# Kernel tuning notes

Hardware: AMD Instinct MI355X
Metric: run time of the kernel (lower is better)

Reference implementation:

```python
import jax, jax.numpy as jnp
import numpy as np
import math

B, L, D_IN = 4, 8192, 64
H = 256          # d_model
N2 = 32          # d_state // 2 complex conjugate pairs (S4D)
NL = 4           # n_layers
D_OUT = 10


def setup_inputs() -> dict:
    key = jax.random.key(0)
    ks = jax.random.split(key, 16)
    x = jax.random.normal(ks[0], (B, L, D_IN), dtype=jnp.float32)
    # encoder Linear(d_input, d_model)
    enc_W = jax.random.normal(ks[1], (H, D_IN), dtype=jnp.float32) / np.sqrt(D_IN)
    enc_b = jnp.zeros((H,), dtype=jnp.float32)
    # per-layer S4D parameters (stacked over n_layers)
    log_dt = jax.random.uniform(ks[2], (NL, H), dtype=jnp.float32,
                                minval=math.log(1e-3), maxval=math.log(1e-1))
    log_A_re = jnp.full((NL, H, N2), math.log(0.5), dtype=jnp.float32)
    A_im = jnp.tile(math.pi * jnp.arange(N2, dtype=jnp.float32), (NL, H, 1))
    C_re = jax.random.normal(ks[3], (NL, H, N2), dtype=jnp.float32) * (0.5 ** 0.5)
    C_im = jax.random.normal(ks[4], (NL, H, N2), dtype=jnp.float32) * (0.5 ** 0.5)
    D = jax.random.normal(ks[5], (NL, H), dtype=jnp.float32)
    # S4 block output linear (H -> 2H) followed by GLU
    Wo = jax.random.normal(ks[6], (NL, 2 * H, H), dtype=jnp.float32) / np.sqrt(H)
    bo = jnp.zeros((NL, 2 * H), dtype=jnp.float32)
    # post-norm LayerNorm over d_model
    ln_w = jnp.ones((NL, H), dtype=jnp.float32)
    ln_b = jnp.zeros((NL, H), dtype=jnp.float32)
    # final decoder Linear(d_model, d_output)
    out_W = jax.random.normal(ks[7], (D_OUT, H), dtype=jnp.float32) / np.sqrt(H)
    out_b = jnp.zeros((D_OUT,), dtype=jnp.float32)
    return dict(x=x, enc_W=enc_W, enc_b=enc_b, log_dt=log_dt, log_A_re=log_A_re,
                A_im=A_im, C_re=C_re, C_im=C_im, D=D, Wo=Wo, bo=bo,
                ln_w=ln_w, ln_b=ln_b, out_W=out_W, out_b=out_b)


def _s4d_kernel(log_dt, log_A_re, A_im, C_re, C_im, L):
    # S4D-ZOH-ish (S4D-Lin) kernel: K[h,l] = 2 Re sum_n C~[h,n] exp(l*dt*A[h,n])
    dt = jnp.exp(log_dt)[:, None]                      # (H,1)
    A = -jnp.exp(log_A_re) + 1j * A_im                 # (H,N2)
    dtA = dt * A                                       # (H,N2)
    Ct = (C_re + 1j * C_im) * (jnp.exp(dtA) - 1.0) / A # (H,N2)
    t = jnp.arange(L, dtype=jnp.float32)
    V = jnp.exp(dtA[:, :, None] * t)                   # (H,N2,L) Vandermonde
    return 2.0 * jnp.einsum('hn,hnl->hl', Ct, V).real  # (H,L)


def reference(x, enc_W, enc_b, log_dt, log_A_re, A_im, C_re, C_im, D, Wo, bo,
              ln_w, ln_b, out_W, out_b):
    Bc, Lc, _ = x.shape
    h = x @ enc_W.T + enc_b          # (B,L,H)
    h = h.transpose(0, 2, 1)         # (B,H,L) (transposed layout)
    n_layers = log_dt.shape[0]
    for i in range(n_layers):
        K = _s4d_kernel(log_dt[i], log_A_re[i], A_im[i], C_re[i], C_im[i], Lc)
        # FFT convolution (causal, non-circular via 2L padding)
        Kf = jnp.fft.rfft(K, n=2 * Lc)                       # (H, L+1)
        hf = jnp.fft.rfft(h, n=2 * Lc)                       # (B,H,L+1)
        y = jnp.fft.irfft(hf * Kf, n=2 * Lc)[..., :Lc]
        y = y + D[i][:, None] * h                            # skip D*u
        y = jax.nn.gelu(y)
        # output linear (H -> 2H) + GLU, pointwise over length
        u = jnp.einsum('oh,bhl->bol', Wo[i], y) + bo[i][:, None]
        Hd = h.shape[1]
        z = u[:, :Hd] * jax.nn.sigmoid(u[:, Hd:])
        h = z + h                                            # residual
        # post-norm LayerNorm over channel (d_model) dim
        mu = h.mean(axis=1, keepdims=True)
        var = h.var(axis=1, keepdims=True)
        h = (h - mu) / jnp.sqrt(var + 1e-5) * ln_w[i][:, None] + ln_b[i][:, None]
    h = h.transpose(0, 2, 1)          # (B,L,H)
    return h @ out_W.T + out_b        # (B,L,d_output)
```

## Files before the change

### kernel.cpp

```cpp
#include <hip/hip_runtime.h>
#include <hip/hip_bf16.h>


constexpr int B_ = 4, L_ = 8192, DIN = 64, H_ = 256, N2_ = 32, NL_ = 4, DOUT = 10;
constexpr int LC = 64, CHK = L_ / LC;
constexpr int GCH = B_ * CHK;
constexpr int M_ = B_ * L_;

constexpr size_t OFF_WOB  = 8388608;
constexpr size_t OFF_PW   = 8650752;
constexpr size_t OFF_PCT  = 8716288;
constexpr size_t OFF_PWLC = 8781824;
constexpr size_t OFF_PZ   = 8847360;
constexpr size_t OFF_EWT  = 8912896;
constexpr size_t OFF_UCM  = 8929280;
constexpr size_t OFF_YCM  = 13123584;
constexpr size_t OFF_MT   = 21512192;
constexpr size_t OFF_MW   = 22036480;
constexpr size_t OFF_MV   = 22560768;

typedef short bf16x8 __attribute__((ext_vector_type(8)));
typedef short short8 __attribute__((ext_vector_type(8)));
typedef float f32x4  __attribute__((ext_vector_type(4)));
typedef int   int2v  __attribute__((ext_vector_type(2)));

__device__ __forceinline__ float b2f(short s) {
    union { float f; unsigned u; } c;
    c.u = ((unsigned)(unsigned short)s) << 16;
    return c.f;
}

__global__ __launch_bounds__(256) void k_params(
    const float* __restrict__ log_dt, const float* __restrict__ log_A_re,
    const float* __restrict__ A_im, const float* __restrict__ C_re,
    const float* __restrict__ C_im, float* __restrict__ ws)
{
    int idx = blockIdx.x * 256 + threadIdx.x;
    if (idx >= NL_ * H_ * N2_) return;
    int i  = idx / (H_ * N2_);
    int hh = (idx / N2_) % H_;
    float dt  = expf(log_dt[i * H_ + hh]);
    float Are = -expf(log_A_re[idx]);
    float Aim = A_im[idx];
    float zre = dt * Are, zim = dt * Aim;
    float er  = expf(zre);
    float wre = er * cosf(zim), wim = er * sinf(zim);
    float d   = Are * Are + Aim * Aim;
    float nre = wre - 1.f, nim = wim;
    float qre = (nre * Are + nim * Aim) / d;
    float qim = (nim * Are - nre * Aim) / d;
    float cr = C_re[idx], ci = C_im[idx];
    float ctre = cr * qre - ci * qim;
    float ctim = cr * qim + ci * qre;
    float er2 = expf(zre * (float)LC);
    float wlre = er2 * cosf(zim * (float)LC);
    float wlim = er2 * sinf(zim * (float)LC);
    ((float2*)(ws + OFF_PW))[idx]   = make_float2(wre, wim);
    ((float2*)(ws + OFF_PCT))[idx]  = make_float2(2.f * ctre, 2.f * ctim);
    ((float2*)(ws + OFF_PWLC))[idx] = make_float2(wlre, wlim);
    ((float2*)(ws + OFF_PZ))[idx]   = make_float2(zre, zim);
}

__global__ __launch_bounds__(256) void k_mats(const float* __restrict__ ws,
    int layer, __hip_bfloat16* __restrict__ mt, __hip_bfloat16* __restrict__ mw,
    __hip_bfloat16* __restrict__ mv)
{
    int h = blockIdx.x, tid = threadIdx.x;
    __shared__ float zre[32], zim[32], ctr[32], cti[32], kv[64];
    if (tid < 32) {
        float2 z = ((const float2*)(ws + OFF_PZ))[(size_t)layer*H_*N2_ + h*N2_ + tid];
        float2 c = ((const float2*)(ws + OFF_PCT))[(size_t)layer*H_*N2_ + h*N2_ + tid];
        zre[tid] = z.x; zim[tid] = z.y; ctr[tid] = c.x; cti[tid] = c.y;
    }
    __syncthreads();
    if (tid < 64) {
        float d = (float)tid, acc = 0.f;
        for (int n = 0; n < 32; n++) {
            float er = expf(zre[n] * d);
            float co = cosf(zim[n] * d), si = sinf(zim[n] * d);
            acc += er * (ctr[n] * co - cti[n] * si);
        }
        kv[tid] = acc;
    }
    __syncthreads();
    {
        int t = tid >> 2, j0 = (tid & 3) * 16;
        alignas(16) __hip_bfloat16 row[16];
        #pragma unroll
        for (int jj = 0; jj < 16; jj++) {
            int j = j0 + jj;
            row[jj] = __float2bfloat16(j <= t ? kv[t - j] : 0.f);
        }
        *(short8*)(mt + (size_t)h*4096 + t*64 + j0)     = *(short8*)&row[0];
        *(short8*)(mt + (size_t)h*4096 + t*64 + j0 + 8) = *(short8*)&row[8];
    }
    {
        int n = tid >> 3, j0 = (tid & 7) * 8;
        alignas(16) __hip_bfloat16 rre[8], rim[8];
        #pragma unroll
        for (int jj = 0; jj < 8; jj++) {
            float e = (float)(63 - (j0 + jj));
            float er = expf(zre[n] * e);
            rre[jj] = __float2bfloat16(er * cosf(zim[n] * e));
            rim[jj] = __float2bfloat16(er * sinf(zim[n] * e));
        }
        *(short8*)(mw + (size_t)h*4096 + (2*n)*64 + j0)   = *(short8*)&rre[0];
        *(short8*)(mw + (size_t)h*4096 + (2*n+1)*64 + j0) = *(short8*)&rim[0];
    }
    {
        int t = tid >> 2, n0 = (tid & 3) * 8;
        float e = (float)(t + 1);
        alignas(16) __hip_bfloat16 row[16];
        #pragma unroll
        for (int k = 0; k < 8; k++) {
            int n = n0 + k;
            float er = expf(zre[n] * e);
            float wr = er * cosf(zim[n] * e), wi = er * sinf(zim[n] * e);
            row[2*k]   = __float2bfloat16(ctr[n]*wr - cti[n]*wi);
            row[2*k+1] = __float2bfloat16(-(ctr[n]*wi + cti[n]*wr));
        }
        *(short8*)(mv + (size_t)h*4096 + t*64 + 2*n0)     = *(short8*)&row[0];
        *(short8*)(mv + (size_t)h*4096 + t*64 + 2*n0 + 8) = *(short8*)&row[8];
    }
}

__global__ __launch_bounds__(256) void k_transpose(const float* __restrict__ src,
    float* __restrict__ dst, int R, int Cc)
{
    __shared__ float t[32][33];
    int x = blockIdx.x * 32 + threadIdx.x;
    #pragma unroll
    for (int i = 0; i < 4; i++) {
        int yy = blockIdx.y * 32 + threadIdx.y + i * 8;
        if (x < Cc && yy < R) t[threadIdx.y + i * 8][threadIdx.x] = src[(size_t)yy * Cc + x];
    }
    __syncthreads();
    int xo = blockIdx.y * 32 + threadIdx.x;
    #pragma unroll
    for (int i = 0; i < 4; i++) {
        int yo = blockIdx.x * 32 + threadIdx.y + i * 8;
        if (xo < R && yo < Cc) dst[(size_t)yo * R + xo] = t[threadIdx.x][threadIdx.y + i * 8];
    }
}

__global__ __launch_bounds__(256) void k_wcvt(const float* __restrict__ src,
    __hip_bfloat16* __restrict__ dst, int n4)
{
    int i = blockIdx.x * 256 + threadIdx.x;
    if (i >= n4) return;
    float4 v = ((const float4*)src)[i];
    union { __hip_bfloat16 b[4]; uint2 u; } o;
    o.b[0] = __float2bfloat16(v.x); o.b[1] = __float2bfloat16(v.y);
    o.b[2] = __float2bfloat16(v.z); o.b[3] = __float2bfloat16(v.w);
    ((uint2*)dst)[i] = o.u;
}

__global__ __launch_bounds__(256) void k_encoder(const float* __restrict__ x,
    const float* __restrict__ encWT, const float* __restrict__ enc_b,
    __hip_bfloat16* __restrict__ u)
{
    __shared__ float As[DIN][36];
    __shared__ float Bs[32][268];
    int m0e = blockIdx.x * 32;
    int tid = threadIdx.x;
    const float4* x4 = (const float4*)x;
    #pragma unroll
    for (int q = 0; q < 2; q++) {
        int f = tid * 2 + q;
        int row = f >> 4, kq = f & 15;
        float4 v = x4[(size_t)(m0e + row) * 16 + kq];
        As[kq * 4 + 0][row] = v.x; As[kq * 4 + 1][row] = v.y;
        As[kq * 4 + 2][row] = v.z; As[kq * 4 + 3][row] = v.w;
    }
    int tx = tid & 31, ty = tid >> 5;
    float acc[4][8];
    #pragma unroll
    for (int p = 0; p < 4; p++)
        #pragma unroll
        for (int j = 0; j < 8; j++) acc[p][j] = 0.f;
    const float4* w4 = (const float4*)encWT;
    for (int ks = 0; ks < 2; ks++) {
        __syncthreads();
        #pragma unroll
        for (int it = 0; it < 8; it++) {
            int q = it * 256 + tid;
            int row = q >> 6, c4 = q & 63;
            *(float4*)&Bs[row][c4 * 4] = w4[ks * 2048 + q];
        }
        __syncthreads();
        #pragma unroll 8
        for (int kk = 0; kk < 32; kk++) {
            int k = ks * 32 + kk;
            float4 a  = *(const float4*)&As[k][ty * 4];
            float4 b0 = *(const float4*)&Bs[kk][tx * 4];
            float4 b1 = *(const float4*)&Bs[kk][128 + tx * 4];
            float av[4] = {a.x, a.y, a.z, a.w};
            float bv[8] = {b0.x, b0.y, b0.z, b0.w, b1.x, b1.y, b1.z, b1.w};
            #pragma unroll
            for (int p = 0; p < 4; p++)
                #pragma unroll
                for (int j = 0; j < 8; j++)
                    acc[p][j] = fmaf(av[p], bv[j], acc[p][j]);
        }
    }
    float4 eb0 = *(const float4*)&enc_b[tx * 4];
    float4 eb1 = *(const float4*)&enc_b[128 + tx * 4];
    float ebv[8] = {eb0.x, eb0.y, eb0.z, eb0.w, eb1.x, eb1.y, eb1.z, eb1.w};
    __syncthreads();
    #pragma unroll
    for (int p = 0; p < 4; p++) {
        int pl = ty * 4 + p;
        #pragma unroll
        for (int j = 0; j < 4; j++) Bs[pl][tx * 4 + j]       = acc[p][j] + ebv[j];
        #pragma unroll
        for (int j = 0; j < 4; j++) Bs[pl][128 + tx * 4 + j] = acc[p][j + 4] + ebv[j + 4];
    }
    __syncthreads();
    {
        alignas(16) __hip_bfloat16 row[32];
        #pragma unroll
        for (int pl = 0; pl < 32; pl++) row[pl] = __float2bfloat16(Bs[pl][tid]);
        #pragma unroll
        for (int q = 0; q < 4; q++)
            *(short8*)(u + (size_t)tid * M_ + m0e + q * 8) = *(short8*)&row[q * 8];
    }
}

__global__ __launch_bounds__(256) void k_ssm(const __hip_bfloat16* __restrict__ ucm,
    const __hip_bfloat16* __restrict__ mt, const __hip_bfloat16* __restrict__ mw,
    const __hip_bfloat16* __restrict__ mv, const float* __restrict__ ws, int layer,
    const float* __restrict__ Dp, __hip_bfloat16* __restrict__ ycm)
{
    __shared__ __hip_bfloat16 ulds[L_];
    __shared__ __hip_bfloat16 st[CHK * 64];
    __shared__ float segT[8][32][2];
    int h = blockIdx.x >> 2, b = blockIdx.x & 3;
    int tid = threadIdx.x, w = tid >> 6, l = tid & 63, l15 = l & 15, l4 = l >> 4;
    const __hip_bfloat16* ub = ucm + (size_t)h * M_ + (size_t)b * L_;
    #pragma unroll
    for (int it = 0; it < 4; it++) {
        int e0 = it * 2048 + tid * 8;
        short8 v = *(const short8*)(ub + e0);
        int c = e0 >> 6, e = e0 & 63;
        *(short8*)&ulds[c * 64 + (e ^ ((c & 7) << 3))] = v;
    }
    __syncthreads();
    {
        const __hip_bfloat16* bbase = mw + (size_t)h * 4096 + l15 * 64 + l4 * 8;
        #pragma unroll
        for (int half = 0; half < 2; half++) {
            int g0 = (w + half * 4) * 16;
            int ca = g0 + l15;
            f32x4 acc[4];
            #pragma unroll
            for (int nj = 0; nj < 4; nj++) acc[nj] = (f32x4)0.f;
            #pragma unroll
            for (int ks = 0; ks < 2; ks++) {
                int e = l4 * 8 + ks * 32;
                bf16x8 a = *(const bf16x8*)&ulds[ca * 64 + (e ^ ((ca & 7) << 3))];
                #pragma unroll
                for (int nj = 0; nj < 4; nj++) {
                    bf16x8 bb = *(const bf16x8*)(bbase + nj * 16 * 64 + ks * 32);
                    acc[nj] = __builtin_amdgcn_mfma_f32_16x16x32_bf16(a, bb, acc[nj], 0, 0, 0);
                }
            }
            #pragma unroll
            for (int nj = 0; nj < 4; nj++)
                #pragma unroll
                for (int r = 0; r < 4; r++) {
                    int c = g0 + l4 * 4 + r, e = nj * 16 + l15;
                    st[c * 64 + (e ^ ((c & 7) << 3))] = __float2bfloat16(acc[nj][r]);
                }
        }
    }
    __syncthreads();
    {
        int s = tid >> 5, n = tid & 31;
        float2 wl = ((const float2*)(ws + OFF_PWLC))[(size_t)layer * H_ * N2_ + h * 32 + n];
        float tr = 0.f, ti = 0.f;
        for (int j = 0; j < 16; j++) {
            int c = s * 16 + j;
            __hip_bfloat162* p = (__hip_bfloat162*)&st[c * 64 + ((2 * n) ^ ((c & 7) << 3))];
            float2 v = __bfloat1622float2(*p);
            float nr = fmaf(wl.x, tr, v.x); nr = fmaf(-wl.y, ti, nr);
            float ni = fmaf(wl.x, ti, v.y); ni = fmaf(wl.y, tr, ni);
            tr = nr; ti = ni;
        }
        segT[s][n][0] = tr; segT[s][n][1] = ti;
        __syncthreads();
        float wr = wl.x, wi = wl.y;
        #pragma unroll
        for (int q = 0; q < 4; q++) {
            float nr = wr * wr - wi * wi, ni = 2.f * wr * wi;
            wr = nr; wi = ni;
        }
        float ar = 0.f, ai = 0.f;
        for (int t = 0; t < s; t++) {
            float Tx = segT[t][n][0], Ty = segT[t][n][1];
            float nr = fmaf(wr, ar, Tx); nr = fmaf(-wi, ai, nr);
            float ni = fmaf(wr, ai, Ty); ni = fmaf(wi, ar, ni);
            ar = nr; ai = ni;
        }
        for (int j = 0; j < 16; j++) {
            int c = s * 16 + j;
            __hip_bfloat162* p = (__hip_bfloat162*)&st[c * 64 + ((2 * n) ^ ((c & 7) << 3))];
            float2 v = __bfloat1622float2(*p);
            *p = __float22bfloat162_rn(make_float2(ar, ai));
            float nr = fmaf(wl.x, ar, v.x); nr = fmaf(-wl.y, ai, nr);
            float ni = fmaf(wl.x, ai, v.y); ni = fmaf(wl.y, ar, ni);
            ar = nr; ai = ni;
        }
    }
    __syncthreads();
    {
        const __hip_bfloat16* bt = mt + (size_t)h * 4096 + l15 * 64 + l4 * 8;
        const __hip_bfloat16* bv = mv + (size_t)h * 4096 + l15 * 64 + l4 * 8;
        float Dh = Dp[layer * H_ + h];
        __hip_bfloat16* yb = ycm + (size_t)h * M_ + (size_t)b * L_;
        #pragma unroll
        for (int half = 0; half < 2; half++) {
            int g0 = (w + half * 4) * 16;
            int ca = g0 + l15;
            f32x4 acc[4];
            #pragma unroll
            for (int nj = 0; nj < 4; nj++) acc[nj] = (f32x4)0.f;
            #pragma unroll
            for (int ks = 0; ks < 2; ks++) {
                int e = l4 * 8 + ks * 32;
                bf16x8 a = *(const bf16x8*)&ulds[ca * 64 + (e ^ ((ca & 7) << 3))];
                #pragma unroll
                for (int nj = 0; nj < 4; nj++) {
                    bf16x8 bb = *(const bf16x8*)(bt + nj * 16 * 64 + ks * 32);
                    acc[nj] = __builtin_amdgcn_mfma_f32_16x16x32_bf16(a, bb, acc[nj], 0, 0, 0);
                }
            }
            #pragma unroll
            for (int ks = 0; ks < 2; ks++) {
                int e = l4 * 8 + ks * 32;
                bf16x8 a = *(const bf16x8*)&st[ca * 64 + (e ^ ((ca & 7) << 3))];
                #pragma unroll
                for (int nj = 0; nj < 4; nj++) {
                    bf16x8 bb = *(const bf16x8*)(bv + nj * 16 * 64 + ks * 32);
                    acc[nj] = __builtin_amdgcn_mfma_f32_16x16x32_bf16(a, bb, acc[nj], 0, 0, 0);
                }
            }
            #pragma unroll
            for (int nj = 0; nj < 4; nj++)
                #pragma unroll
                for (int r = 0; r < 4; r++) {
                    int g = g0 + l4 * 4 + r;
                    int e = nj * 16 + l15;
                    float uv = __bfloat162float(ulds[g * 64 + (e ^ ((g & 7) << 3))]);
                    float v = fmaf(Dh, uv, acc[nj][r]);
                    float gg = 0.7978845608028654f * fmaf(0.044715f * v, v * v, v);
                    float yv = v / (1.f + __expf(-2.f * gg));
                    yb[(size_t)g * 64 + nj * 16 + l15] = __float2bfloat16(yv);
                }
        }
    }
}

__global__ __launch_bounds__(256) void k_glu_mfma(
    const __hip_bfloat16* __restrict__ ycm,
    const __hip_bfloat16* __restrict__ wob,
    const float* __restrict__ bo, const float* __restrict__ lnw,
    const float* __restrict__ lnb,
    __hip_bfloat16* __restrict__ u)
{
    __shared__ int buf[8320];
    __shared__ float red[4][32][2];
    int* bufA = buf;
    int* bufR = buf + 4160;
    int tid = threadIdx.x;
    int w = tid >> 6, l = tid & 63, l15 = l & 15, l4 = l >> 4;
    int mb = blockIdx.x * 64;
    int nv = w * 64;
    int p = tid & 127, ph = tid >> 7;
    const __hip_bfloat16* aB = ycm + (size_t)(2 * p) * M_ + mb + ph * 16;
    const __hip_bfloat16* rB = u + (size_t)(2 * p) * M_ + mb + ph * 16;

    short8 A0[4], R0[4], A1[4], R1[4];
    A0[0] = *(const short8*)(aB);          A0[1] = *(const short8*)(aB + 8);
    A0[2] = *(const short8*)(aB + M_);     A0[3] = *(const short8*)(aB + M_ + 8);
    R0[0] = *(const short8*)(rB);          R0[1] = *(const short8*)(rB + 8);
    R0[2] = *(const short8*)(rB + M_);     R0[3] = *(const short8*)(rB + M_ + 8);
    A1[0] = *(const short8*)(aB + 32);     A1[1] = *(const short8*)(aB + 40);
    A1[2] = *(const short8*)(aB + M_ + 32);A1[3] = *(const short8*)(aB + M_ + 40);

    float bov[4], bog[4], lw[4], lb[4];
    #pragma unroll
    for (int nj = 0; nj < 4; nj++) {
        int cn = nv + nj * 16 + l15;
        bov[nj] = bo[cn]; bog[nj] = bo[256 + cn];
        lw[nj] = lnw[cn]; lb[nj] = lnb[cn];
    }

    {
        int* da = bufA + ph * 16 * 130 + p;
        int* dr = bufR + ph * 16 * 130 + p;
        #pragma unroll
        for (int j = 0; j < 8; j++) {
            da[j * 130]       = ((int)(unsigned short)A0[0][j]) | (((int)(unsigned short)A0[2][j]) << 16);
            da[(8 + j) * 130] = ((int)(unsigned short)A0[1][j]) | (((int)(unsigned short)A0[3][j]) << 16);
            dr[j * 130]       = ((int)(unsigned short)R0[0][j]) | (((int)(unsigned short)R0[2][j]) << 16);
            dr[(8 + j) * 130] = ((int)(unsigned short)R0[1][j]) | (((int)(unsigned short)R0[3][j]) << 16);
        }
    }
    __syncthreads();

    int abase0 = l15 * 130 + l4 * 4;
    #pragma unroll
    for (int tile = 0; tile < 2; tile++) {
        int m0 = mb + tile * 32;
        f32x4 accv[2][4], accg[2][4];
        #pragma unroll
        for (int sub = 0; sub < 2; sub++)
            #pragma unroll
            for (int nj = 0; nj < 4; nj++) { accv[sub][nj] = (f32x4)0.f; accg[sub][nj] = (f32x4)0.f; }

        #pragma unroll 2
        for (int ks = 0; ks < 8; ks++) {
            int k0 = ks * 32 + l4 * 8;
            union { int2v d[2]; bf16x8 v; } a0u, a1u;
            a0u.d[0] = *(const int2v*)&bufA[abase0 + ks * 16];
            a0u.d[1] = *(const int2v*)&bufA[abase0 + ks * 16 + 2];
            a1u.d[0] = *(const int2v*)&bufA[abase0 + 16 * 130 + ks * 16];
            a1u.d[1] = *(const int2v*)&bufA[abase0 + 16 * 130 + ks * 16 + 2];
            bf16x8 a0 = a0u.v;
            bf16x8 a1 = a1u.v;
            #pragma unroll
            for (int nj = 0; nj < 4; nj++) {
                bf16x8 bv = *(const bf16x8*)(wob + (size_t)(nv + nj * 16 + l15) * H_ + k0);
                bf16x8 bg = *(const bf16x8*)(wob + (size_t)(256 + nv + nj * 16 + l15) * H_ + k0);
                accv[0][nj] = __builtin_amdgcn_mfma_f32_16x16x32_bf16(a0, bv, accv[0][nj], 0, 0, 0);
                accg[0][nj] = __builtin_amdgcn_mfma_f32_16x16x32_bf16(a0, bg, accg[0][nj], 0, 0, 0);
                accv[1][nj] = __builtin_amdgcn_mfma_f32_16x16x32_bf16(a1, bv, accv[1][nj], 0, 0, 0);
                accg[1][nj] = __builtin_amdgcn_mfma_f32_16x16x32_bf16(a1, bg, accg[1][nj], 0, 0, 0);
            }
        }

        const short* bufRs = (const short*)bufR;
        #pragma unroll
        for (int sub = 0; sub < 2; sub++) {
            #pragma unroll
            for (int r = 0; r < 4; r++) {
                int lr = sub * 16 + l4 * 4 + r;
                float s = 0.f, ss = 0.f;
                #pragma unroll
                for (int nj = 0; nj < 4; nj++) {
                    int cn = nv + nj * 16 + l15;
                    float uv = accv[sub][nj][r] + bov[nj];
                    float ug = accg[sub][nj][r] + bog[nj];
                    float z = uv / (1.f + __expf(-ug));
                    float v = z + b2f(bufRs[lr * 260 + cn]);
                    accv[sub][nj][r] = v;
                    s += v; ss += v * v;
                }
                #pragma unroll
                for (int off = 1; off < 16; off <<= 1) {
                    s  += __shfl_xor(s, off);
                    ss += __shfl_xor(ss, off);
                }
                if (l15 == 0) { red[w][lr][0] = s; red[w][lr][1] = ss; }
            }
        }
        if (tile == 0) {
            R1[0] = *(const short8*)(rB + 32);      R1[1] = *(const short8*)(rB + 40);
            R1[2] = *(const short8*)(rB + M_ + 32); R1[3] = *(const short8*)(rB + M_ + 40);
        }
        __syncthreads();
        short* lt = (short*)buf;
        #pragma unroll
        for (int sub = 0; sub < 2; sub++) {
            #pragma unroll
            for (int r = 0; r < 4; r++) {
                int lr = sub * 16 + l4 * 4 + r;
                float s  = red[0][lr][0] + red[1][lr][0] + red[2][lr][0] + red[3][lr][0];
                float ss = red[0][lr][1] + red[1][lr][1] + red[2][lr][1] + red[3][lr][1];
                float mu = s * (1.f / 256.f);
                float var = ss * (1.f / 256.f) - mu * mu;
                float rstd = rsqrtf(var + 1e-5f);
                #pragma unroll
                for (int nj = 0; nj < 4; nj++) {
                    int cn = nv + nj * 16 + l15;
                    float val = (accv[sub][nj][r] - mu) * rstd * lw[nj] + lb[nj];
                    __hip_bfloat16 bval = __float2bfloat16(val);
                    lt[cn * 34 + lr] = *(short*)&bval;
                }
            }
        }
        __syncthreads();
        #pragma unroll
        for (int q = 0; q < 4; q++)
            *(short8*)(u + (size_t)tid * M_ + m0 + q * 8)
                = *(short8*)&lt[tid * 34 + q * 8];
        if (tile == 0) {
            __syncthreads();
            int* da = bufA + ph * 16 * 130 + p;
            int* dr = bufR + ph * 16 * 130 + p;
            #pragma unroll
            for (int j = 0; j < 8; j++) {
                da[j * 130]       = ((int)(unsigned short)A1[0][j]) | (((int)(unsigned short)A1[2][j]) << 16);
                da[(8 + j) * 130] = ((int)(unsigned short)A1[1][j]) | (((int)(unsigned short)A1[3][j]) << 16);
                dr[j * 130]       = ((int)(unsigned short)R1[0][j]) | (((int)(unsigned short)R1[2][j]) << 16);
                dr[(8 + j) * 130] = ((int)(unsigned short)R1[1][j]) | (((int)(unsigned short)R1[3][j]) << 16);
            }
            __syncthreads();
        }
    }
}

__global__ __launch_bounds__(256) void k_decoder(const __hip_bfloat16* __restrict__ u,
    const float* __restrict__ out_W, const float* __restrict__ out_b,
    float* __restrict__ out)
{
    __shared__ int ds[64 * 130];
    __shared__ float wl[10][260];
    int m0 = blockIdx.x * 64;
    int tid = threadIdx.x;
    {
        int p = tid & 127, ph = tid >> 7;
        const __hip_bfloat16* s0 = u + (size_t)(2 * p) * M_ + m0 + ph * 32;
        const __hip_bfloat16* s1 = s0 + M_;
        short8 y0[4], y1[4];
        #pragma unroll
        for (int q = 0; q < 4; q++) {
            y0[q] = *(const short8*)(s0 + q * 8);
            y1[q] = *(const short8*)(s1 + q * 8);
        }
        int* dst = ds + (ph * 32) * 130 + p;
        #pragma unroll
        for (int q = 0; q < 4; q++)
            #pragma unroll
            for (int j = 0; j < 8; j++)
                dst[(q * 8 + j) * 130] =
                    ((int)(unsigned short)y0[q][j]) | (((int)(unsigned short)y1[q][j]) << 16);
    }
    for (int q = tid; q < 640; q += 256) {
        int r = q / 64, k4 = q % 64;
        *(float4*)&wl[r][k4 * 4] = ((const float4*)out_W)[q];
    }
    __syncthreads();
    int slot = tid & 15;
    if (slot < DOUT) {
        #pragma unroll
        for (int pass = 0; pass < 4; pass++) {
            int pl = pass * 16 + (tid >> 4);
            const int* row = ds + pl * 130;
            float a0 = 0.f, a1 = 0.f;
            #pragma unroll 8
            for (int d = 0; d < 128; d++) {
                int v = row[d];
                a0 = fmaf(b2f((short)(v & 0xffff)),  wl[slot][2 * d],     a0);
                a1 = fmaf(b2f((short)(v >> 16)),     wl[slot][2 * d + 1], a1);
            }
            out[(size_t)(m0 + pl) * DOUT + slot] = a0 + a1 + out_b[slot];
        }
    }
}

extern "C" void kernel_launch(void* const* d_in, const int* in_sizes, int n_in,
                              void* d_out, int out_size, void* d_ws, size_t ws_size,
                              hipStream_t stream)
{
    (void)in_sizes; (void)n_in; (void)out_size; (void)ws_size;
    const float* x        = (const float*)d_in[0];
    const float* enc_W    = (const float*)d_in[1];
    const float* enc_b    = (const float*)d_in[2];
    const float* log_dt   = (const float*)d_in[3];
    const float* log_A_re = (const float*)d_in[4];
    const float* A_im     = (const float*)d_in[5];
    const float* C_re     = (const float*)d_in[6];
    const float* C_im     = (const float*)d_in[7];
    const float* Dp       = (const float*)d_in[8];
    const float* Wo       = (const float*)d_in[9];
    const float* bo       = (const float*)d_in[10];
    const float* lnw      = (const float*)d_in[11];
    const float* lnb      = (const float*)d_in[12];
    const float* out_W    = (const float*)d_in[13];
    const float* out_b    = (const float*)d_in[14];
    float* ws = (float*)d_ws;
    __hip_bfloat16* u   = (__hip_bfloat16*)(ws + OFF_UCM);
    __hip_bfloat16* ycm = (__hip_bfloat16*)(ws + OFF_YCM);
    __hip_bfloat16* mt = (__hip_bfloat16*)(ws + OFF_MT);
    __hip_bfloat16* mw = (__hip_bfloat16*)(ws + OFF_MW);
    __hip_bfloat16* mv = (__hip_bfloat16*)(ws + OFF_MV);
    __hip_bfloat16* wob = (__hip_bfloat16*)(ws + OFF_WOB);

    k_params<<<NL_ * H_ * N2_ / 256, 256, 0, stream>>>(log_dt, log_A_re, A_im, C_re, C_im, ws);
    dim3 tb(32, 8);
    k_transpose<<<dim3(DIN / 32, H_ / 32), tb, 0, stream>>>(enc_W, ws + OFF_EWT, H_, DIN);
    k_wcvt<<<(NL_ * 2 * H_ * H_ / 4 + 255) / 256, 256, 0, stream>>>(Wo, wob, NL_ * 2 * H_ * H_ / 4);
    k_encoder<<<M_ / 32, 256, 0, stream>>>(x, ws + OFF_EWT, enc_b, u);
    for (int i = 0; i < NL_; i++) {
        k_mats<<<H_, 256, 0, stream>>>(ws, i, mt, mw, mv);
        k_ssm<<<H_ * B_, 256, 0, stream>>>(u, mt, mw, mv, ws, i, Dp, ycm);
        k_glu_mfma<<<M_ / 64, 256, 0, stream>>>(ycm,
            wob + (size_t)i * 2 * H_ * H_, bo + (size_t)i * 2 * H_,
            lnw + (size_t)i * H_, lnb + (size_t)i * H_, u);
    }
    k_decoder<<<M_ / 64, 256, 0, stream>>>(u, out_W, out_b, (float*)d_out);
}
```

Before: 418.8 us.

## Use bf16 MFMA for encoder and batch SSM matrix generation across layers

```diff
diff --git a/kernel.cpp b/kernel.cpp
--- a/kernel.cpp
+++ b/kernel.cpp
@@ -7,17 +7,18 @@
 constexpr int GCH = B_ * CHK;
 constexpr int M_ = B_ * L_;
 
+constexpr size_t OFF_XB   = 0;
+constexpr size_t OFF_EWB  = 1048576;
 constexpr size_t OFF_WOB  = 8388608;
 constexpr size_t OFF_PW   = 8650752;
 constexpr size_t OFF_PCT  = 8716288;
 constexpr size_t OFF_PWLC = 8781824;
 constexpr size_t OFF_PZ   = 8847360;
-constexpr size_t OFF_EWT  = 8912896;
 constexpr size_t OFF_UCM  = 8929280;
 constexpr size_t OFF_YCM  = 13123584;
-constexpr size_t OFF_MT   = 21512192;
-constexpr size_t OFF_MW   = 22036480;
-constexpr size_t OFF_MV   = 22560768;
+constexpr size_t OFF_MTA  = 17317888;
+constexpr size_t OFF_MWA  = 19415040;
+constexpr size_t OFF_MVA  = 21512192;
 
 typedef short bf16x8 __attribute__((ext_vector_type(8)));
 typedef short short8 __attribute__((ext_vector_type(8)));
@@ -61,15 +62,18 @@
     ((float2*)(ws + OFF_PZ))[idx]   = make_float2(zre, zim);
 }
 
-__global__ __launch_bounds__(256) void k_mats(const float* __restrict__ ws,
-    int layer, __hip_bfloat16* __restrict__ mt, __hip_bfloat16* __restrict__ mw,
+__global__ __launch_bounds__(256) void k_mats_all(const float* __restrict__ ws,
+    __hip_bfloat16* __restrict__ mt, __hip_bfloat16* __restrict__ mw,
     __hip_bfloat16* __restrict__ mv)
 {
-    int h = blockIdx.x, tid = threadIdx.x;
+    int bid = blockIdx.x;
+    int layer = bid >> 8, h = bid & 255;
+    int lh = layer * H_ + h;
+    int tid = threadIdx.x;
     __shared__ float zre[32], zim[32], ctr[32], cti[32], kv[64];
     if (tid < 32) {
-        float2 z = ((const float2*)(ws + OFF_PZ))[(size_t)layer*H_*N2_ + h*N2_ + tid];
-        float2 c = ((const float2*)(ws + OFF_PCT))[(size_t)layer*H_*N2_ + h*N2_ + tid];
+        float2 z = ((const float2*)(ws + OFF_PZ))[(size_t)lh * N2_ + tid];
+        float2 c = ((const float2*)(ws + OFF_PCT))[(size_t)lh * N2_ + tid];
         zre[tid] = z.x; zim[tid] = z.y; ctr[tid] = c.x; cti[tid] = c.y;
     }
     __syncthreads();
@@ -91,8 +95,8 @@
             int j = j0 + jj;
             row[jj] = __float2bfloat16(j <= t ? kv[t - j] : 0.f);
         }
-        *(short8*)(mt + (size_t)h*4096 + t*64 + j0)     = *(short8*)&row[0];
-        *(short8*)(mt + (size_t)h*4096 + t*64 + j0 + 8) = *(short8*)&row[8];
+        *(short8*)(mt + (size_t)lh*4096 + t*64 + j0)     = *(short8*)&row[0];
+        *(short8*)(mt + (size_t)lh*4096 + t*64 + j0 + 8) = *(short8*)&row[8];
     }
     {
         int n = tid >> 3, j0 = (tid & 7) * 8;
@@ -104,8 +108,8 @@
             rre[jj] = __float2bfloat16(er * cosf(zim[n] * e));
             rim[jj] = __float2bfloat16(er * sinf(zim[n] * e));
         }
-        *(short8*)(mw + (size_t)h*4096 + (2*n)*64 + j0)   = *(short8*)&rre[0];
-        *(short8*)(mw + (size_t)h*4096 + (2*n+1)*64 + j0) = *(short8*)&rim[0];
+        *(short8*)(mw + (size_t)lh*4096 + (2*n)*64 + j0)   = *(short8*)&rre[0];
+        *(short8*)(mw + (size_t)lh*4096 + (2*n+1)*64 + j0) = *(short8*)&rim[0];
     }
     {
         int t = tid >> 2, n0 = (tid & 3) * 8;
@@ -119,27 +123,8 @@
             row[2*k]   = __float2bfloat16(ctr[n]*wr - cti[n]*wi);
             row[2*k+1] = __float2bfloat16(-(ctr[n]*wi + cti[n]*wr));
         }
-        *(short8*)(mv + (size_t)h*4096 + t*64 + 2*n0)     = *(short8*)&row[0];
-        *(short8*)(mv + (size_t)h*4096 + t*64 + 2*n0 + 8) = *(short8*)&row[8];
-    }
-}
-
-__global__ __launch_bounds__(256) void k_transpose(const float* __restrict__ src,
-    float* __restrict__ dst, int R, int Cc)
-{
-    __shared__ float t[32][33];
-    int x = blockIdx.x * 32 + threadIdx.x;
-    #pragma unroll
-    for (int i = 0; i < 4; i++) {
-        int yy = blockIdx.y * 32 + threadIdx.y + i * 8;
-        if (x < Cc && yy < R) t[threadIdx.y + i * 8][threadIdx.x] = src[(size_t)yy * Cc + x];
-    }
-    __syncthreads();
-    int xo = blockIdx.y * 32 + threadIdx.x;
-    #pragma unroll
-    for (int i = 0; i < 4; i++) {
-        int yo = blockIdx.x * 32 + threadIdx.y + i * 8;
-        if (xo < R && yo < Cc) dst[(size_t)yo * R + xo] = t[threadIdx.x][threadIdx.y + i * 8];
+        *(short8*)(mv + (size_t)lh*4096 + t*64 + 2*n0)     = *(short8*)&row[0];
+        *(short8*)(mv + (size_t)lh*4096 + t*64 + 2*n0 + 8) = *(short8*)&row[8];
     }
 }
 
@@ -155,75 +140,54 @@
     ((uint2*)dst)[i] = o.u;
 }
 
-__global__ __launch_bounds__(256) void k_encoder(const float* __restrict__ x,
-    const float* __restrict__ encWT, const float* __restrict__ enc_b,
+__global__ __launch_bounds__(256) void k_encoder(const __hip_bfloat16* __restrict__ xb,
+    const __hip_bfloat16* __restrict__ ewb, const float* __restrict__ enc_b,
     __hip_bfloat16* __restrict__ u)
 {
-    __shared__ float As[DIN][36];
-    __shared__ float Bs[32][268];
-    int m0e = blockIdx.x * 32;
+    __shared__ short lt[256 * 66];
     int tid = threadIdx.x;
-    const float4* x4 = (const float4*)x;
-    #pragma unroll
-    for (int q = 0; q < 2; q++) {
-        int f = tid * 2 + q;
-        int row = f >> 4, kq = f & 15;
-        float4 v = x4[(size_t)(m0e + row) * 16 + kq];
-        As[kq * 4 + 0][row] = v.x; As[kq * 4 + 1][row] = v.y;
-        As[kq * 4 + 2][row] = v.z; As[kq * 4 + 3][row] = v.w;
-    }
-    int tx = tid & 31, ty = tid >> 5;
-    float acc[4][8];
-    #pragma unroll
-    for (int p = 0; p < 4; p++)
-        #pragma unroll
-        for (int j = 0; j < 8; j++) acc[p][j] = 0.f;
-    const float4* w4 = (const float4*)encWT;
+    int w = tid >> 6, l = tid & 63, l15 = l & 15, l4 = l >> 4;
+    int m0 = blockIdx.x * 64;
+    int nv = w * 64;
+    f32x4 acc[4][4];
+    #pragma unroll
+    for (int mi = 0; mi < 4; mi++)
+        #pragma unroll
+        for (int nj = 0; nj < 4; nj++) acc[mi][nj] = (f32x4)0.f;
+    #pragma unroll
     for (int ks = 0; ks < 2; ks++) {
-        __syncthreads();
-        #pragma unroll
-        for (int it = 0; it < 8; it++) {
-            int q = it * 256 + tid;
-            int row = q >> 6, c4 = q & 63;
-            *(float4*)&Bs[row][c4 * 4] = w4[ks * 2048 + q];
-        }
-        __syncthreads();
-        #pragma unroll 8
-        for (int kk = 0; kk < 32; kk++) {
-            int k = ks * 32 + kk;
-            float4 a  = *(const float4*)&As[k][ty * 4];
-            float4 b0 = *(const float4*)&Bs[kk][tx * 4];
-            float4 b1 = *(const float4*)&Bs[kk][128 + tx * 4];
-            float av[4] = {a.x, a.y, a.z, a.w};
-            float bv[8] = {b0.x, b0.y, b0.z, b0.w, b1.x, b1.y, b1.z, b1.w};
-            #pragma unroll
-            for (int p = 0; p < 4; p++)
-                #pragma unroll
-                for (int j = 0; j < 8; j++)
-                    acc[p][j] = fmaf(av[p], bv[j], acc[p][j]);
-        }
-    }
-    float4 eb0 = *(const float4*)&enc_b[tx * 4];
-    float4 eb1 = *(const float4*)&enc_b[128 + tx * 4];
-    float ebv[8] = {eb0.x, eb0.y, eb0.z, eb0.w, eb1.x, eb1.y, eb1.z, eb1.w};
-    __syncthreads();
-    #pragma unroll
-    for (int p = 0; p < 4; p++) {
-        int pl = ty * 4 + p;
-        #pragma unroll
-        for (int j = 0; j < 4; j++) Bs[pl][tx * 4 + j]       = acc[p][j] + ebv[j];
-        #pragma unroll
-        for (int j = 0; j < 4; j++) Bs[pl][128 + tx * 4 + j] = acc[p][j + 4] + ebv[j + 4];
-    }
-    __syncthreads();
-    {
-        alignas(16) __hip_bfloat16 row[32];
-        #pragma unroll
-        for (int pl = 0; pl < 32; pl++) row[pl] = __float2bfloat16(Bs[pl][tid]);
-        #pragma unroll
-        for (int q = 0; q < 4; q++)
-            *(short8*)(u + (size_t)tid * M_ + m0e + q * 8) = *(short8*)&row[q * 8];
-    }
+        int k0 = ks * 32 + l4 * 8;
+        bf16x8 a[4];
+        #pragma unroll
+        for (int mi = 0; mi < 4; mi++)
+            a[mi] = *(const bf16x8*)(xb + (size_t)(m0 + mi * 16 + l15) * 64 + k0);
+        #pragma unroll
+        for (int nj = 0; nj < 4; nj++) {
+            bf16x8 b = *(const bf16x8*)(ewb + (size_t)(nv + nj * 16 + l15) * 64 + k0);
+            #pragma unroll
+            for (int mi = 0; mi < 4; mi++)
+                acc[mi][nj] = __builtin_amdgcn_mfma_f32_16x16x32_bf16(a[mi], b, acc[mi][nj], 0, 0, 0);
+        }
+    }
+    float bov[4];
+    #pragma unroll
+    for (int nj = 0; nj < 4; nj++) bov[nj] = enc_b[nv + nj * 16 + l15];
+    #pragma unroll
+    for (int mi = 0; mi < 4; mi++)
+        #pragma unroll
+        for (int r = 0; r < 4; r++) {
+            int lr = mi * 16 + l4 * 4 + r;
+            #pragma unroll
+            for (int nj = 0; nj < 4; nj++) {
+                int cn = nv + nj * 16 + l15;
+                __hip_bfloat16 bv = __float2bfloat16(acc[mi][nj][r] + bov[nj]);
+                lt[cn * 66 + lr] = *(short*)&bv;
+            }
+        }
+    __syncthreads();
+    #pragma unroll
+    for (int q = 0; q < 8; q++)
+        *(short8*)(u + (size_t)tid * M_ + m0 + q * 8) = *(short8*)&lt[tid * 66 + q * 8];
 }
 
 __global__ __launch_bounds__(256) void k_ssm(const __hip_bfloat16* __restrict__ ucm,
@@ -580,21 +544,25 @@
     const float* out_W    = (const float*)d_in[13];
     const float* out_b    = (const float*)d_in[14];
     float* ws = (float*)d_ws;
+    __hip_bfloat16* xb  = (__hip_bfloat16*)(ws + OFF_XB);
+    __hip_bfloat16* ewb = (__hip_bfloat16*)(ws + OFF_EWB);
     __hip_bfloat16* u   = (__hip_bfloat16*)(ws + OFF_UCM);
     __hip_bfloat16* ycm = (__hip_bfloat16*)(ws + OFF_YCM);
-    __hip_bfloat16* mt = (__hip_bfloat16*)(ws + OFF_MT);
-    __hip_bfloat16* mw = (__hip_bfloat16*)(ws + OFF_MW);
-    __hip_bfloat16* mv = (__hip_bfloat16*)(ws + OFF_MV);
+    __hip_bfloat16* mtA = (__hip_bfloat16*)(ws + OFF_MTA);
+    __hip_bfloat16* mwA = (__hip_bfloat16*)(ws + OFF_MWA);
+    __hip_bfloat16* mvA = (__hip_bfloat16*)(ws + OFF_MVA);
     __hip_bfloat16* wob = (__hip_bfloat16*)(ws + OFF_WOB);
 
     k_params<<<NL_ * H_ * N2_ / 256, 256, 0, stream>>>(log_dt, log_A_re, A_im, C_re, C_im, ws);
-    dim3 tb(32, 8);
-    k_transpose<<<dim3(DIN / 32, H_ / 32), tb, 0, stream>>>(enc_W, ws + OFF_EWT, H_, DIN);
     k_wcvt<<<(NL_ * 2 * H_ * H_ / 4 + 255) / 256, 256, 0, stream>>>(Wo, wob, NL_ * 2 * H_ * H_ / 4);
-    k_encoder<<<M_ / 32, 256, 0, stream>>>(x, ws + OFF_EWT, enc_b, u);
+    k_wcvt<<<(M_ * DIN / 4 + 255) / 256, 256, 0, stream>>>(x, xb, M_ * DIN / 4);
+    k_wcvt<<<(H_ * DIN / 4 + 255) / 256, 256, 0, stream>>>(enc_W, ewb, H_ * DIN / 4);
+    k_mats_all<<<NL_ * H_, 256, 0, stream>>>(ws, mtA, mwA, mvA);
+    k_encoder<<<M_ / 64, 256, 0, stream>>>(xb, ewb, enc_b, u);
     for (int i = 0; i < NL_; i++) {
-        k_mats<<<H_, 256, 0, stream>>>(ws, i, mt, mw, mv);
-        k_ssm<<<H_ * B_, 256, 0, stream>>>(u, mt, mw, mv, ws, i, Dp, ycm);
+        k_ssm<<<H_ * B_, 256, 0, stream>>>(u,
+            mtA + (size_t)i * H_ * 4096, mwA + (size_t)i * H_ * 4096,
+            mvA + (size_t)i * H_ * 4096, ws, i, Dp, ycm);
         k_glu_mfma<<<M_ / 64, 256, 0, stream>>>(ycm,
             wob + (size_t)i * 2 * H_ * H_, bo + (size_t)i * 2 * H_,
             lnw + (size_t)i * H_, lnb + (size_t)i * H_, u);
```

Result: faster. 366.5 us (-12.5%).
